# Performance work log

Measured on AMD Instinct MI355X. Metric: run time of the kernel, lower is better.

## Reference

```python
import jax, jax.numpy as jnp
import numpy as np

B, H, S, D = 4, 12, 2048, 64

def setup_inputs() -> dict:
    key = jax.random.key(0)
    kq, kk, kv, km = jax.random.split(key, 4)
    q = jax.random.normal(kq, (B, H, S, D), dtype=jnp.float32)
    k = jax.random.normal(kk, (B, H, S, D), dtype=jnp.float32)
    v = jax.random.normal(kv, (B, H, S, D), dtype=jnp.float32)
    # key padding mask: True = masked out, broadcastable to [B,H,S,S]
    key_padding_mask = jax.random.randint(km, (B, 1, 1, S), 0, 2).astype(bool)
    return {"q": q, "k": k, "v": v, "key_padding_mask": key_padding_mask}

def reference(q, k, v, key_padding_mask):
    d_k = q.shape[-1]
    # [B,H,S,S] logits, scaled
    attn_logits = jnp.einsum("bhqd,bhkd->bhqk", q, k) / jnp.sqrt(jnp.float32(d_k))
    # masked_fill(key_padding_mask, -inf)
    attn_logits = jnp.where(key_padding_mask, -jnp.inf, attn_logits)
    attention = jax.nn.softmax(attn_logits, axis=-1)
    values = jnp.einsum("bhqk,bhkd->bhqd", attention, v)
    return values, attn_logits
```

## Files before the change

### kernel.cpp

```cpp
#include <hip/hip_runtime.h>
#include <hip/hip_bf16.h>

#define Bz 4
#define Hh 12
#define Ss 2048
#define Dd 64
#define KT 64
#define NT (Ss / KT)

#define MASK_NEG (-1.0e30f)

typedef _Float16 f16x8 __attribute__((ext_vector_type(8)));
typedef float f32x4 __attribute__((ext_vector_type(4)));

#define LDK (Dd + 8)
#define LDP (KT + 8)

#define LGKM_BARRIER() do { \
    asm volatile("s_waitcnt lgkmcnt(0)" ::: "memory"); \
    __builtin_amdgcn_s_barrier(); \
} while (0)

__device__ __forceinline__ int vswz(int d) { return (d ^ (d >> 2)) & 7; }

__global__ __launch_bounds__(256)
void attn_fwd(const float* __restrict__ qg, const float* __restrict__ kg,
              const float* __restrict__ vg, const unsigned char* __restrict__ maskg,
              float* __restrict__ out_vals, float* __restrict__ out_logits)
{
    __shared__ __align__(16) _Float16 K_lds[KT][LDK];
    __shared__ __align__(16) _Float16 Vt_lds[Dd * 64];
    __shared__ __align__(16) _Float16 P_lds[4][16][LDP];

    int cpx = gridDim.x >> 3;
    int bid = blockIdx.x;
    int o   = (bid & 7) * cpx + (bid >> 3);
    int bh  = o >> 5;
    int qt  = o & 31;
    int b   = bh / Hh;

    int tid  = threadIdx.x;
    int wave = tid >> 6;
    int lane = tid & 63;
    int lo   = lane & 15;
    int hi   = lane >> 4;

    const float* qbase = qg + (size_t)bh * Ss * Dd;
    const float* kbase = kg + (size_t)bh * Ss * Dd;
    const float* vbase = vg + (size_t)bh * Ss * Dd;
    const unsigned char* mbase = maskg + (size_t)b * Ss;

    int q0   = qt * 64;
    int qrow = q0 + wave * 16 + lo;

    int srow = tid >> 4;
    int sc4  = tid & 15;

    f16x8 qf[2];
    #pragma unroll
    for (int c = 0; c < 2; ++c) {
        const float* p = qbase + (size_t)qrow * Dd + c * 32 + hi * 8;
        f32x4 a0 = *(const f32x4*)p;
        f32x4 a1 = *(const f32x4*)(p + 4);
        f16x8 t;
        t[0]=(_Float16)a0[0]; t[1]=(_Float16)a0[1]; t[2]=(_Float16)a0[2]; t[3]=(_Float16)a0[3];
        t[4]=(_Float16)a1[0]; t[5]=(_Float16)a1[1]; t[6]=(_Float16)a1[2]; t[7]=(_Float16)a1[3];
        qf[c] = t;
    }

    f32x4 o_acc[4] = {};
    float l_acc[4] = {0.0f, 0.0f, 0.0f, 0.0f};

    f32x4 kq[4], vq[4];
    #pragma unroll
    for (int i = 0; i < 4; ++i) {
        int row = srow + i * 16;
        kq[i] = *(const f32x4*)(kbase + (size_t)row * Dd + sc4 * 4);
        vq[i] = *(const f32x4*)(vbase + (size_t)row * Dd + sc4 * 4);
    }

    for (int ktile = 0; ktile < NT; ++ktile) {
        int k0 = ktile * KT;

        #pragma unroll
        for (int i = 0; i < 4; ++i) {
            int row = srow + i * 16;
            _Float16* kp = &K_lds[row][sc4 * 4];
            kp[0]=(_Float16)kq[i][0]; kp[1]=(_Float16)kq[i][1];
            kp[2]=(_Float16)kq[i][2]; kp[3]=(_Float16)kq[i][3];
            int kb = row >> 3, kl = row & 7;
            #pragma unroll
            for (int j = 0; j < 4; ++j) {
                int d = sc4 * 4 + j;
                Vt_lds[d * 64 + ((kb ^ vswz(d)) << 3) + kl] = (_Float16)vq[i][j];
            }
        }
        LGKM_BARRIER();

        if (ktile + 1 < NT) {
            int kn0 = (ktile + 1) * KT;
            #pragma unroll
            for (int i = 0; i < 4; ++i) {
                int row = srow + i * 16;
                kq[i] = *(const f32x4*)(kbase + (size_t)(kn0 + row) * Dd + sc4 * 4);
                vq[i] = *(const f32x4*)(vbase + (size_t)(kn0 + row) * Dd + sc4 * 4);
            }
        }

        f32x4 s[4];
        #pragma unroll
        for (int n = 0; n < 4; ++n) {
            f16x8 kf0 = *(const f16x8*)&K_lds[n*16 + lo][      hi*8];
            f16x8 kf1 = *(const f16x8*)&K_lds[n*16 + lo][32 + hi*8];
            f32x4 acc = {};
            acc = __builtin_amdgcn_mfma_f32_16x16x32_f16(qf[0], kf0, acc, 0, 0, 0);
            acc = __builtin_amdgcn_mfma_f32_16x16x32_f16(qf[1], kf1, acc, 0, 0, 0);
            s[n] = acc;
        }

        int grow0 = q0 + wave * 16 + hi * 4;
        #pragma unroll
        for (int n = 0; n < 4; ++n) {
            int col = k0 + n * 16 + lo;
            bool msk = mbase[col] != 0;
            #pragma unroll
            for (int r = 0; r < 4; ++r) {
                float sv = s[n][r] * 0.125f;
                sv = msk ? MASK_NEG : sv;
                __builtin_nontemporal_store(sv,
                    &out_logits[(size_t)(bh * Ss + grow0 + r) * Ss + col]);
                float p = __expf(sv);
                l_acc[r] += p;
                P_lds[wave][hi*4 + r][n*16 + lo] = (_Float16)p;
            }
        }

        f16x8 pf0 = *(const f16x8*)&P_lds[wave][lo][      hi*8];
        f16x8 pf1 = *(const f16x8*)&P_lds[wave][lo][32 + hi*8];
        #pragma unroll
        for (int n0 = 0; n0 < 4; ++n0) {
            int d0 = n0*16 + lo;
            int sw = vswz(d0);
            f16x8 vf0 = *(const f16x8*)&Vt_lds[d0*64 + (((    hi) ^ sw) << 3)];
            f16x8 vf1 = *(const f16x8*)&Vt_lds[d0*64 + (((4 + hi) ^ sw) << 3)];
            o_acc[n0] = __builtin_amdgcn_mfma_f32_16x16x32_f16(pf0, vf0, o_acc[n0], 0, 0, 0);
            o_acc[n0] = __builtin_amdgcn_mfma_f32_16x16x32_f16(pf1, vf1, o_acc[n0], 0, 0, 0);
        }

        LGKM_BARRIER();
    }

    #pragma unroll
    for (int r = 0; r < 4; ++r) {
        float x = l_acc[r];
        x += __shfl_xor(x, 1);
        x += __shfl_xor(x, 2);
        x += __shfl_xor(x, 4);
        x += __shfl_xor(x, 8);
        l_acc[r] = x;
    }

    int grow0 = q0 + wave * 16 + hi * 4;
    #pragma unroll
    for (int r = 0; r < 4; ++r) {
        float inv = 1.0f / l_acc[r];
        #pragma unroll
        for (int n0 = 0; n0 < 4; ++n0) {
            float val = o_acc[n0][r] * inv;
            __builtin_nontemporal_store(val,
                &out_vals[(size_t)(bh * Ss + grow0 + r) * Dd + n0*16 + lo]);
        }
    }
}

extern "C" void kernel_launch(void* const* d_in, const int* in_sizes, int n_in,
                              void* d_out, int out_size, void* d_ws, size_t ws_size,
                              hipStream_t stream) {
    const float* q = (const float*)d_in[0];
    const float* k = (const float*)d_in[1];
    const float* v = (const float*)d_in[2];
    const unsigned char* mask = (const unsigned char*)d_in[3];

    float* out_vals   = (float*)d_out;
    float* out_logits = out_vals + (size_t)Bz * Hh * Ss * Dd;

    int grid = Bz * Hh * (Ss / 64);
    attn_fwd<<<grid, 256, 0, stream>>>(q, k, v, mask, out_vals, out_logits);
}
```

Baseline: 261.7 us.

## Transpose MFMA operand order so each lane writes contiguous logits as float4

Swaps the A/B operands of both MFMA products so the accumulator holds the transposed tile. Each lane then owns four consecutive key columns of one query row. Logits and output values can be written as 16-byte nontemporal vector stores instead of scalar stores, and the mask is read as one 32-bit word. The row-sum reduction becomes a single scalar with two cross-lane shuffles. The change targets the store-bound cost of writing the large logits tensor, at the price of 8-byte P writes into LDS that may cause bank conflicts.

```diff
diff --git a/kernel.cpp b/kernel.cpp
--- a/kernel.cpp
+++ b/kernel.cpp
@@ -11,6 +11,7 @@
 #define MASK_NEG (-1.0e30f)
 
 typedef _Float16 f16x8 __attribute__((ext_vector_type(8)));
+typedef _Float16 f16x4 __attribute__((ext_vector_type(4)));
 typedef float f32x4 __attribute__((ext_vector_type(4)));
 
 #define LDK (Dd + 8)
@@ -69,7 +70,7 @@
     }
 
     f32x4 o_acc[4] = {};
-    float l_acc[4] = {0.0f, 0.0f, 0.0f, 0.0f};
+    float l_acc = 0.0f;
 
     f32x4 kq[4], vq[4];
     #pragma unroll
@@ -113,26 +114,30 @@
             f16x8 kf0 = *(const f16x8*)&K_lds[n*16 + lo][      hi*8];
             f16x8 kf1 = *(const f16x8*)&K_lds[n*16 + lo][32 + hi*8];
             f32x4 acc = {};
-            acc = __builtin_amdgcn_mfma_f32_16x16x32_f16(qf[0], kf0, acc, 0, 0, 0);
-            acc = __builtin_amdgcn_mfma_f32_16x16x32_f16(qf[1], kf1, acc, 0, 0, 0);
+            acc = __builtin_amdgcn_mfma_f32_16x16x32_f16(kf0, qf[0], acc, 0, 0, 0);
+            acc = __builtin_amdgcn_mfma_f32_16x16x32_f16(kf1, qf[1], acc, 0, 0, 0);
             s[n] = acc;
         }
 
-        int grow0 = q0 + wave * 16 + hi * 4;
+        size_t lrow = ((size_t)bh * Ss + qrow) * Ss + k0;
         #pragma unroll
         for (int n = 0; n < 4; ++n) {
-            int col = k0 + n * 16 + lo;
-            bool msk = mbase[col] != 0;
+            unsigned mw = *(const unsigned*)&mbase[k0 + n*16 + hi*4];
+            f32x4 sv;
             #pragma unroll
             for (int r = 0; r < 4; ++r) {
-                float sv = s[n][r] * 0.125f;
-                sv = msk ? MASK_NEG : sv;
-                __builtin_nontemporal_store(sv,
-                    &out_logits[(size_t)(bh * Ss + grow0 + r) * Ss + col]);
-                float p = __expf(sv);
-                l_acc[r] += p;
-                P_lds[wave][hi*4 + r][n*16 + lo] = (_Float16)p;
+                float x = s[n][r] * 0.125f;
+                sv[r] = ((mw >> (8*r)) & 255u) ? MASK_NEG : x;
             }
+            __builtin_nontemporal_store(sv, (f32x4*)&out_logits[lrow + n*16 + hi*4]);
+            f16x4 ph;
+            #pragma unroll
+            for (int r = 0; r < 4; ++r) {
+                float p = __expf(sv[r]);
+                l_acc += p;
+                ph[r] = (_Float16)p;
+            }
+            *(f16x4*)&P_lds[wave][lo][n*16 + hi*4] = ph;
         }
 
         f16x8 pf0 = *(const f16x8*)&P_lds[wave][lo][      hi*8];
@@ -143,33 +148,24 @@
             int sw = vswz(d0);
             f16x8 vf0 = *(const f16x8*)&Vt_lds[d0*64 + (((    hi) ^ sw) << 3)];
             f16x8 vf1 = *(const f16x8*)&Vt_lds[d0*64 + (((4 + hi) ^ sw) << 3)];
-            o_acc[n0] = __builtin_amdgcn_mfma_f32_16x16x32_f16(pf0, vf0, o_acc[n0], 0, 0, 0);
-            o_acc[n0] = __builtin_amdgcn_mfma_f32_16x16x32_f16(pf1, vf1, o_acc[n0], 0, 0, 0);
+            o_acc[n0] = __builtin_amdgcn_mfma_f32_16x16x32_f16(vf0, pf0, o_acc[n0], 0, 0, 0);
+            o_acc[n0] = __builtin_amdgcn_mfma_f32_16x16x32_f16(vf1, pf1, o_acc[n0], 0, 0, 0);
         }
 
         LGKM_BARRIER();
     }
 
+    l_acc += __shfl_xor(l_acc, 16);
+    l_acc += __shfl_xor(l_acc, 32);
+    float inv = 1.0f / l_acc;
+
     #pragma unroll
-    for (int r = 0; r < 4; ++r) {
-        float x = l_acc[r];
-        x += __shfl_xor(x, 1);
-        x += __shfl_xor(x, 2);
-        x += __shfl_xor(x, 4);
-        x += __shfl_xor(x, 8);
-        l_acc[r] = x;
-    }
-
-    int grow0 = q0 + wave * 16 + hi * 4;
-    #pragma unroll
-    for (int r = 0; r < 4; ++r) {
-        float inv = 1.0f / l_acc[r];
+    for (int n0 = 0; n0 < 4; ++n0) {
+        f32x4 ov;
         #pragma unroll
-        for (int n0 = 0; n0 < 4; ++n0) {
-            float val = o_acc[n0][r] * inv;
-            __builtin_nontemporal_store(val,
-                &out_vals[(size_t)(bh * Ss + grow0 + r) * Dd + n0*16 + lo]);
-        }
+        for (int r = 0; r < 4; ++r) ov[r] = o_acc[n0][r] * inv;
+        __builtin_nontemporal_store(ov,
+            (f32x4*)&out_vals[((size_t)bh * Ss + qrow) * Dd + n0*16 + hi*4]);
     }
 }
 
```

Result: faster. 254.3 us (-2.8%).
